# Optimization experiments

Measured on AMD Instinct MI355X. Metric: run time of the kernel, lower is better.

## Reference

```python
import jax, jax.numpy as jnp
import numpy as np


def _blur_kernel():
    # make_kernel([1,3,3,1]) -> outer product, normalized; * upsample_factor**2 (=4)
    k = np.array([1.0, 3.0, 3.0, 1.0], dtype=np.float32)
    k2 = np.outer(k, k)
    k2 /= k2.sum()
    k2 *= 4.0
    return jnp.asarray(k2)  # [4,4]


def setup_inputs() -> dict:
    key = jax.random.key(0)
    ks = jax.random.split(key, 6)
    B, Cin, Cout, H, W = 8, 128, 128, 128, 128
    style_dim, sd = 512, 32
    lin_out = Cin * (sd // 2) * (sd // 2)  # 128*16*16 = 32768
    return {
        "x": jax.random.normal(ks[0], (B, Cin, H, W), jnp.float32),
        "style": jax.random.normal(ks[1], (B, style_dim), jnp.float32),
        "weight": jax.random.normal(ks[2], (Cout, Cin, 3, 3), jnp.float32),
        "lin_w": jax.random.normal(ks[3], (lin_out, style_dim), jnp.float32),
        "lin_b": jnp.ones((lin_out,), jnp.float32),  # bias_init=1
        "convw_w": jax.random.normal(ks[4], (Cout, Cin, 3, 3), jnp.float32),
        "convw_b": jnp.zeros((Cout,), jnp.float32),
        "convb_w": jax.random.normal(ks[5], (Cout, Cin, 3, 3), jnp.float32),
        "convb_b": jnp.zeros((Cout,), jnp.float32),
    }


DN = ('NCHW', 'OIHW', 'NCHW')


def reference(x, style, weight, lin_w, lin_b, convw_w, convw_b, convb_w, convb_b):
    B, Cin, H, W = x.shape
    Cout, K = weight.shape[0], weight.shape[2]
    scale = 1.0 / np.sqrt(Cin * K * K)  # equalized-lr scale, fan_in = Cin*K*K
    w = scale * weight  # [Cout, Cin, K, K]; identical per-sample -> plain conv

    # F.conv_transpose2d(stride=2, padding=0) == dilated conv with flipped kernel
    out = jax.lax.conv_general_dilated(
        x, jnp.flip(w, (2, 3)), (1, 1), [(K - 1, K - 1)] * 2,
        lhs_dilation=(2, 2), dimension_numbers=DN)  # [B, Cout, 2H+1, 2W+1]

    # upfirdn2d blur with pad=(1,1): depthwise conv with flipped 4x4 kernel
    bk = _blur_kernel()
    bw = jnp.tile(jnp.flip(bk, (0, 1))[None, None], (Cout, 1, 1, 1))  # [Cout,1,4,4]
    out = jax.lax.conv_general_dilated(
        out, bw, (1, 1), [(1, 1), (1, 1)], feature_group_count=Cout,
        dimension_numbers=DN)  # [B, Cout, 2H, 2W]

    # InstanceNorm2d(affine=False), eps=1e-5, biased variance
    mu = out.mean((2, 3), keepdims=True)
    var = out.var((2, 3), keepdims=True)
    out = (out - mu) * jax.lax.rsqrt(var + 1e-5)
    Ho, Wo = out.shape[2], out.shape[3]

    # spatial_modulation_shared: EqualLinear (fused_lrelu) + View
    half = int(round(np.sqrt(lin_w.shape[0] // Cin)))  # spatial_dim // 2
    sd = 2 * half
    lscale = 1.0 / np.sqrt(style.shape[1])
    s = style @ (lin_w * lscale).T
    s = jax.nn.leaky_relu(s + lin_b, 0.2) * np.sqrt(2.0)  # fused_leaky_relu
    smap = s.reshape(B, Cin, half, half)
    # nn.Upsample(scale_factor=2, mode='nearest')
    smap = jnp.repeat(jnp.repeat(smap, 2, axis=2), 2, axis=3)  # [B,Cin,sd,sd]

    # two EqualConv2d(Cin, Cout, 3, padding=1)
    cscale = 1.0 / np.sqrt(Cin * 9)
    sw = jax.lax.conv_general_dilated(smap, convw_w * cscale, (1, 1),
                                      [(1, 1), (1, 1)], dimension_numbers=DN)
    sw = sw + convw_b[None, :, None, None]
    sb = jax.lax.conv_general_dilated(smap, convb_w * cscale, (1, 1),
                                      [(1, 1), (1, 1)], dimension_numbers=DN)
    sb = sb + convb_b[None, :, None, None]

    # F.interpolate(mode='nearest') to (Ho, Wo)
    hi = jnp.arange(Ho) * sd // Ho
    wi = jnp.arange(Wo) * sd // Wo
    sw = sw[:, :, hi][:, :, :, wi]
    sb = sb[:, :, hi][:, :, :, wi]

    return out * (1.0 + 0.3 * sw) + 0.3 * sb
```

## Files before the change

kernel.cpp:

```cpp
#include <hip/hip_runtime.h>
#include <cstdint>

#define SCALE_MAIN 0.029462782549439483f
#define LSCALE     0.044194173824159223f
#define CSCALE     0.029462782549439483f

typedef __attribute__((ext_vector_type(8))) short bf16x8;
typedef __attribute__((ext_vector_type(4))) float f32x4;
typedef __attribute__((ext_vector_type(2))) unsigned int u32x2;
typedef __attribute__((ext_vector_type(4))) unsigned int u32x4;

static __device__ __forceinline__ float lrelu_s2(float v) {
  return (v > 0.f ? v : 0.2f * v) * 1.4142135623730951f;
}
static __device__ __forceinline__ unsigned short f2bf(float f) {
  unsigned int u = __builtin_bit_cast(unsigned int, f);
  u += 0x7FFFu + ((u >> 16) & 1u);
  return (unsigned short)(u >> 16);
}
static __device__ __forceinline__ float s2f(unsigned short s) {
  return __builtin_bit_cast(float, (unsigned int)s << 16);
}
static __device__ __forceinline__ float lo16(unsigned int v) {
  return __builtin_bit_cast(float, v << 16);
}
static __device__ __forceinline__ float hi16(unsigned int v) {
  return __builtin_bit_cast(float, v & 0xFFFF0000u);
}

__global__ __launch_bounds__(256) void prep_all(
    const float* __restrict__ weight, const float* __restrict__ cw_w,
    const float* __restrict__ cb_w, const float* __restrict__ x,
    const float* __restrict__ style, const float* __restrict__ lin_w,
    const float* __restrict__ lin_b, short* __restrict__ kbu,
    short* __restrict__ kb2, unsigned short* __restrict__ xt,
    unsigned short* __restrict__ smap_bf) {
  int bid = blockIdx.x;
  int t = threadIdx.x;
  if (bid < 2048) {
    int idx = bid * 256 + t;
    int j   = idx & 7;
    int co  = (idx >> 3) & 255;
    int kc  = (idx >> 11) & 63;
    int par = idx >> 17;
    int k = kc * 8 + j;
    int t2 = k >> 7, ci = k & 127;
    int dy2 = t2 >> 1, dx2 = t2 & 1;
    int ph = par >> 1, pw = par & 1;
    const float* wsrc = (co < 128)
        ? cw_w + ((size_t)co * 128 + ci) * 9
        : cb_w + ((size_t)(co - 128) * 128 + ci) * 9;
    float acc = 0.f;
    #pragma unroll
    for (int kh = 0; kh < 3; ++kh) {
      bool okh = dy2 == 0 ? (ph == 0 ? kh == 0 : kh <= 1)
                          : (ph == 0 ? kh >= 1 : kh == 2);
      if (!okh) continue;
      #pragma unroll
      for (int kw = 0; kw < 3; ++kw) {
        bool okw = dx2 == 0 ? (pw == 0 ? kw == 0 : kw <= 1)
                            : (pw == 0 ? kw >= 1 : kw == 2);
        if (okw) acc += wsrc[kh * 3 + kw];
      }
    }
    kb2[idx] = (short)f2bf(acc * CSCALE);
  } else if (bid < 2624) {
    int idx2 = (bid - 2048) * 256 + t;
    int j    = idx2 & 7;
    int co   = (idx2 >> 3) & 127;
    int ksub = (idx2 >> 10) & 3;
    int s    = (idx2 >> 12) & 3;
    int tp   = idx2 >> 14;
    int ci = s * 32 + ksub * 8 + j;
    int wr = (tp == 0 || tp == 1 || tp == 4) ? 2
           : (tp >= 6) ? 1 : 0;
    int wc = (tp == 0 || tp == 2 || tp == 6) ? 2
           : (tp == 4 || tp == 5 || tp == 8) ? 1 : 0;
    float v = weight[((size_t)(co * 128 + ci)) * 9 + wr * 3 + wc] * SCALE_MAIN;
    kbu[idx2] = (short)f2bf(v);
  } else if (bid < 3648) {
    int q = bid - 2624;
    int y = q & 127, b = q >> 7;
    __shared__ unsigned short tl[128 * 134];
    #pragma unroll 4
    for (int i = 0; i < 16; ++i) {
      int c = t + i * 256;
      int ci = c >> 5, x4 = c & 31;
      f32x4 v = *(const f32x4*)(x + (size_t)(b * 128 + ci) * 16384 + y * 128 + x4 * 4);
      unsigned int* dst = (unsigned int*)(tl + ci * 134 + x4 * 4);
      dst[0] = (unsigned int)f2bf(v.x) | ((unsigned int)f2bf(v.y) << 16);
      dst[1] = (unsigned int)f2bf(v.z) | ((unsigned int)f2bf(v.w) << 16);
    }
    __syncthreads();
    #pragma unroll 2
    for (int i = 0; i < 8; ++i) {
      int c = t + i * 256;
      int xcol = c >> 4, sub = c & 15;
      unsigned short u[8];
      #pragma unroll
      for (int j = 0; j < 8; ++j) u[j] = tl[(sub * 8 + j) * 134 + xcol];
      u32x4 o;
      o.x = (unsigned int)u[0] | ((unsigned int)u[1] << 16);
      o.y = (unsigned int)u[2] | ((unsigned int)u[3] << 16);
      o.z = (unsigned int)u[4] | ((unsigned int)u[5] << 16);
      o.w = (unsigned int)u[6] | ((unsigned int)u[7] << 16);
      *(u32x4*)(xt + ((size_t)(b * 128 + y) * 128 + xcol) * 128 + sub * 8) = o;
    }
  } else {
    int wid = t >> 6, lane = t & 63;
    int gw = (bid - 3648) * 4 + wid;
    const float4* st4 = (const float4*)style;
    float s[8][8];
    #pragma unroll
    for (int b = 0; b < 8; ++b) {
      float4 a0 = st4[b * 128 + lane * 2];
      float4 a1 = st4[b * 128 + lane * 2 + 1];
      s[b][0] = a0.x; s[b][1] = a0.y; s[b][2] = a0.z; s[b][3] = a0.w;
      s[b][4] = a1.x; s[b][5] = a1.y; s[b][6] = a1.z; s[b][7] = a1.w;
    }
    for (int rr = 0; rr < 16; ++rr) {
      int j = gw * 16 + rr;
      const float4* wp = (const float4*)(lin_w + (size_t)j * 512);
      float4 w0 = wp[lane * 2], w1 = wp[lane * 2 + 1];
      float acc[8];
      #pragma unroll
      for (int b = 0; b < 8; ++b) {
        acc[b] = w0.x * s[b][0] + w0.y * s[b][1] + w0.z * s[b][2] + w0.w * s[b][3]
               + w1.x * s[b][4] + w1.y * s[b][5] + w1.z * s[b][6] + w1.w * s[b][7];
      }
      #pragma unroll
      for (int m = 32; m; m >>= 1) {
        #pragma unroll
        for (int b = 0; b < 8; ++b) acc[b] += __shfl_xor(acc[b], m, 64);
      }
      if (lane == 0) {
        float bias = lin_b[j];
        int ci = j >> 8, sp = j & 255;
        #pragma unroll
        for (int b = 0; b < 8; ++b)
          smap_bf[(size_t)(b * 256 + sp) * 128 + ci] =
              f2bf(lrelu_s2(acc[b] * LSCALE + bias));
      }
    }
  }
}

__global__ __launch_bounds__(512, 2) void modconv_kernel(
    const unsigned short* __restrict__ smap_bf, const short* __restrict__ kb2,
    const float* __restrict__ cw_b, const float* __restrict__ cb_b,
    float* __restrict__ swp) {
  extern __shared__ __align__(16) char dsm[];
  int par = blockIdx.x, b = blockIdx.y;
  int ph = par >> 1, pw = par & 1;
  int t = threadIdx.x, lane = t & 63, w = t >> 6;
  int q = w >> 1, ch = w & 1;
  int m15 = lane & 15, ksub = lane >> 4;

  for (int c = t; c < 4624; c += 512) {
    int s = c >> 4, cch = c & 15;
    int rr = s / 17, cc = s - rr * 17;
    int gr = rr - 1 + ph, gc = cc - 1 + pw;
    u32x4 v = {0u, 0u, 0u, 0u};
    if ((unsigned)gr < 16u && (unsigned)gc < 16u)
      v = *(const u32x4*)(smap_bf + ((size_t)(b * 256 + gr * 16 + gc) * 128 + cch * 8));
    int phys = (cch + s) & 15;
    *(u32x4*)(dsm + s * 256 + phys * 16) = v;
  }
  __syncthreads();

  const bf16x8* kbv = (const bf16x8*)kb2;
  f32x4 acc[4][8];
  #pragma unroll
  for (int i = 0; i < 4; ++i)
  #pragma unroll
  for (int j = 0; j < 8; ++j) acc[i][j] = (f32x4){0.f, 0.f, 0.f, 0.f};

  for (int s = 0; s < 16; ++s) {
    int t2 = s >> 2, dy2 = t2 >> 1, dx2 = t2 & 1;
    int cch = (s & 3) * 4 + ksub;
    bf16x8 av[4];
    #pragma unroll
    for (int mf = 0; mf < 4; ++mf) {
      int i = q * 4 + mf;
      int ssp = (i + dy2) * 17 + (m15 + dx2);
      int phys = (cch + ssp) & 15;
      av[mf] = *(const bf16x8*)(dsm + ssp * 256 + phys * 16);
    }
    #pragma unroll
    for (int nf = 0; nf < 8; ++nf) {
      bf16x8 bv = kbv[(size_t)((par * 64 + s * 4 + ksub) * 256 + ch * 128 + nf * 16 + m15)];
      #pragma unroll
      for (int mf = 0; mf < 4; ++mf)
        acc[mf][nf] = __builtin_amdgcn_mfma_f32_16x16x32_bf16(av[mf], bv, acc[mf][nf], 0, 0, 0);
    }
  }

  int jbase = ksub * 4;
  #pragma unroll
  for (int nf = 0; nf < 8; ++nf) {
    int co = ch * 128 + nf * 16 + m15;
    float bias = (co < 128) ? cw_b[co] : cb_b[co - 128];
    #pragma unroll
    for (int mf = 0; mf < 4; ++mf) {
      int i = q * 4 + mf;
      #pragma unroll
      for (int r = 0; r < 4; ++r) {
        int px = i * 16 + jbase + r;
        swp[((size_t)(b * 256 + co) * 4 + par) * 256 + px] = acc[mf][nf][r] + bias;
      }
    }
  }
}

__global__ __launch_bounds__(256, 2) void convt_kernel(
    const unsigned short* __restrict__ xt, const short* __restrict__ kbu,
    unsigned short* __restrict__ out1) {
  __shared__ __align__(16) char smem[26112];
  int cg = blockIdx.x, rp = blockIdx.y, b = blockIdx.z;
  int t = threadIdx.x, lane = t & 63, w = t >> 6;
  int m15 = lane & 15, ksub = lane >> 4;
  int pl = (w + cg + rp) & 3;
  int tstart = (pl == 0) ? 0 : 2 + 2 * pl;
  int nst = 16 >> ((pl + 1) >> 1);

  const char* xtc = (const char*)xt;
  for (int c = t; c < 1632; c += 256) {
    int spos = c >> 4, sub = c & 15;
    int lr = spos / 34, lc = spos - lr * 34;
    int y = 2 * rp - 1 + lr, xg = 32 * cg - 1 + lc;
    f32x4 v = {0.f, 0.f, 0.f, 0.f};
    if ((unsigned)y < 128u && (unsigned)xg < 128u)
      v = *(const f32x4*)(xtc + ((size_t)((b * 128 + y) * 128 + xg)) * 256 + sub * 16);
    int phys = (sub & 8) | ((sub ^ spos) & 7);
    *(f32x4*)(smem + spos * 256 + phys * 16) = v;
  }
  __syncthreads();

  const bf16x8* kbv = (const bf16x8*)kbu;
  f32x4 acc[4][8];
  #pragma unroll
  for (int i = 0; i < 4; ++i)
  #pragma unroll
  for (int j = 0; j < 8; ++j) acc[i][j] = (f32x4){0.f, 0.f, 0.f, 0.f};

  auto LD = [&](int s, bf16x8* av, bf16x8* bv) {
    int tap = tstart + (s >> 2);
    int du = -((0x13 >> tap) & 1);
    int dv = -((0x45 >> tap) & 1);
    int cc = s & 3;
    int c = cc * 4 + ksub;
    #pragma unroll
    for (int mf = 0; mf < 4; ++mf) {
      int spos = ((mf >> 1) + du + 1) * 34 + (mf & 1) * 16 + m15 + dv + 1;
      int phys = (c & 8) | ((c ^ spos) & 7);
      av[mf] = *(const bf16x8*)(smem + spos * 256 + phys * 16);
    }
    int bb = tap * 2048 + cc * 512 + ksub * 128 + m15;
    #pragma unroll
    for (int nf = 0; nf < 8; ++nf) bv[nf] = kbv[bb + nf * 16];
  };
  auto MM = [&](bf16x8* av, bf16x8* bv) {
    __builtin_amdgcn_s_setprio(1);
    #pragma unroll
    for (int nf = 0; nf < 8; ++nf)
    #pragma unroll
    for (int mf = 0; mf < 4; ++mf)
      acc[mf][nf] = __builtin_amdgcn_mfma_f32_16x16x32_bf16(av[mf], bv[nf], acc[mf][nf], 0, 0, 0);
    __builtin_amdgcn_s_setprio(0);
  };

  bf16x8 aA[4], bA[8], aB[4], bB[8];
  LD(0, aA, bA);
  for (int s = 0; s + 2 <= nst; s += 2) {
    LD(s + 1, aB, bB);
    MM(aA, bA);
    if (s + 2 < nst) LD(s + 2, aA, bA);
    MM(aB, bB);
  }

  __syncthreads();
  float* eps = (float*)smem;
  int t63 = t & 63, wpl = t >> 6;
  #pragma unroll
  for (int nf = 0; nf < 8; ++nf) {
    #pragma unroll
    for (int mf = 0; mf < 4; ++mf)
    #pragma unroll
    for (int r = 0; r < 4; ++r)
      eps[(pl * 64 + mf * 16 + ksub * 4 + r) * 17 + m15] = acc[mf][nf][r];
    __syncthreads();
    #pragma unroll
    for (int k = 0; k < 4; ++k) {
      int slot = k * 64 + t63;
      int co16 = slot >> 4, pr = (slot >> 3) & 1, ch = slot & 7;
      float v0 = eps[(wpl * 64 + pr * 32 + ch * 4 + 0) * 17 + co16];
      float v1 = eps[(wpl * 64 + pr * 32 + ch * 4 + 1) * 17 + co16];
      float v2 = eps[(wpl * 64 + pr * 32 + ch * 4 + 2) * 17 + co16];
      float v3 = eps[(wpl * 64 + pr * 32 + ch * 4 + 3) * 17 + co16];
      u32x2 o;
      o.x = (unsigned int)f2bf(v0) | ((unsigned int)f2bf(v1) << 16);
      o.y = (unsigned int)f2bf(v2) | ((unsigned int)f2bf(v3) << 16);
      int co = nf * 16 + co16;
      int r = 2 * rp + pr;
      size_t ob = (((size_t)(b * 4 + wpl) * 128 + co) * 130 + r) * 132
                + 32 * cg + ch * 4;
      if (cg < 4 || ch == 0) *(u32x2*)(out1 + ob) = o;
    }
    __syncthreads();
  }
}

template <int PASS>
__global__ __launch_bounds__(256) void blur_kernel(
    const unsigned short* __restrict__ out1, float* __restrict__ part,
    const float* __restrict__ swp, float* __restrict__ dout) {
  __shared__ unsigned short S[4][18][132];
  __shared__ float T[32][132];
  __shared__ float lsw[4][32], lsb[4][32];
  __shared__ float msh[2];
  __shared__ float rb2[8];
  int g = blockIdx.x, co = blockIdx.y, b = blockIdx.z;
  int t = threadIdx.x, lane = t & 63, wid = t >> 6;
  int bc = b * 128 + co;

  if (PASS == 1) {
    if (t == 0) {
      float a1 = 0.f, a2 = 0.f;
      #pragma unroll
      for (int i = 0; i < 8; ++i) {
        a1 += part[((size_t)bc * 8 + i) * 2];
        a2 += part[((size_t)bc * 8 + i) * 2 + 1];
      }
      float mean = a1 * (1.f / 65536.f);
      float var = a2 * (1.f / 65536.f) - mean * mean;
      msh[0] = mean; msh[1] = rsqrtf(var + 1e-5f);
    }
    {
      int which = t >> 7;
      int par = (t >> 5) & 3;
      int idx = t & 31;
      int hrow = idx >> 4, wcol = idx & 15;
      int px2 = (2 * g + hrow) * 16 + wcol;
      float v = swp[((size_t)(b * 256 + which * 128 + co) * 4 + par) * 256 + px2];
      if (which == 0) lsw[par][idx] = v; else lsb[par][idx] = v;
    }
  }

  int rbase = 16 * g - 1;
  for (int i = t; i < 2376; i += 256) {
    int pl = i / 594; int rem = i - pl * 594;
    int lr = rem / 33; int lc8 = rem - lr * 33;
    int r = rbase + lr;
    u32x2 v = {0u, 0u};
    if (r >= 0)
      v = *(const u32x2*)(out1 + ((size_t)((b * 4 + pl) * 128 + co) * 130 + r) * 132 + lc8 * 4);
    *(u32x2*)(&S[0][0][0] + (pl * 18 + lr) * 132 + lc8 * 4) = v;
  }
  if (t < 32) T[t][0] = 0.f;
  __syncthreads();

  float mean = 0.f, rstd = 0.f;
  if (PASS == 1) { mean = msh[0]; rstd = msh[1]; }
  float s1 = 0.f, s2 = 0.f;

  #pragma unroll
  for (int half = 0; half < 2; ++half) {
    if (half == 1) __syncthreads();
    if (t < 130) {
      int pw = (t >= 65) ? 1 : 0;
      int pc2 = t - 65 * pw;
      const unsigned int* E = (const unsigned int*)&S[pw][0][0] + pc2;
      const unsigned int* O = (const unsigned int*)&S[2 + pw][0][0] + pc2;
      float* Tr = &T[0][0] + pw * 132 + 2 * pc2 + 1;
      #pragma unroll
      for (int k = 0; k < 16; ++k) {
        int hl = half * 16 + k;
        int lrb = (hl + 1) >> 1;
        float v0, v1;
        if (hl & 1) {
          unsigned int e0 = E[lrb * 66],        o0 = O[lrb * 66];
          unsigned int e1 = E[(lrb + 1) * 66],  o1 = O[(lrb + 1) * 66];
          v0 = (lo16(e0) + lo16(o1)) + 3.f * (lo16(o0) + lo16(e1));
          v1 = (hi16(e0) + hi16(o1)) + 3.f * (hi16(o0) + hi16(e1));
        } else {
          unsigned int o0 = O[lrb * 66];
          unsigned int e1 = E[(lrb + 1) * 66],  o1 = O[(lrb + 1) * 66];
          unsigned int e2 = E[(lrb + 2) * 66];
          v0 = (lo16(o0) + lo16(e2)) + 3.f * (lo16(e1) + lo16(o1));
          v1 = (hi16(o0) + hi16(e2)) + 3.f * (hi16(e1) + hi16(o1));
        }
        Tr[k * 264] = v0;
        Tr[k * 264 + 1] = v1;
      }
    }
    __syncthreads();
    {
      int n = t & 127, hh = t >> 7;
      #pragma unroll
      for (int k = 0; k < 8; ++k) {
        int klocal = k * 2 + hh;
        const float* T0 = &T[klocal * 2][0];
        const float* T1 = &T[klocal * 2 + 1][0];
        float t0n = T0[n], t0n1 = T0[n + 1], t0n2 = T0[n + 2];
        float t1n = T1[n], t1n1 = T1[n + 1], t1n2 = T1[n + 2];
        float ve = ((t1n + t0n2) + 3.f * (t0n1 + t1n1)) * 0.0625f;
        float vo = ((t0n1 + t1n2) + 3.f * (t1n1 + t0n2)) * 0.0625f;
        if (PASS == 0) {
          s1 += ve + vo; s2 += ve * ve + vo * vo;
        } else {
          int hl = half * 16 + klocal;
          int h = 32 * g + hl;
          int par = ((klocal >> 3) & 1) * 2 + ((n >> 2) & 1);
          int lidx = half * 16 + (n >> 3);
          float msw = lsw[par][lidx], msb = lsb[par][lidx];
          float f1 = (1.f + 0.3f * msw) * rstd;
          float f0 = 0.3f * msb - mean * f1;
          float2 o = make_float2(ve * f1 + f0, vo * f1 + f0);
          *(float2*)(dout + ((size_t)bc * 256 + h) * 256 + 2 * n) = o;
        }
      }
    }
  }

  if (PASS == 0) {
    #pragma unroll
    for (int m = 32; m; m >>= 1) { s1 += __shfl_xor(s1, m, 64); s2 += __shfl_xor(s2, m, 64); }
    if (lane == 0) { rb2[wid * 2] = s1; rb2[wid * 2 + 1] = s2; }
    __syncthreads();
    if (t == 0) {
      part[((size_t)bc * 8 + g) * 2]     = rb2[0] + rb2[2] + rb2[4] + rb2[6];
      part[((size_t)bc * 8 + g) * 2 + 1] = rb2[1] + rb2[3] + rb2[5] + rb2[7];
    }
  }
}

extern "C" void kernel_launch(void* const* d_in, const int* in_sizes, int n_in,
                              void* d_out, int out_size, void* d_ws, size_t ws_size,
                              hipStream_t stream) {
  const float* x      = (const float*)d_in[0];
  const float* style  = (const float*)d_in[1];
  const float* weight = (const float*)d_in[2];
  const float* lin_w  = (const float*)d_in[3];
  const float* lin_b  = (const float*)d_in[4];
  const float* cw_w   = (const float*)d_in[5];
  const float* cw_b   = (const float*)d_in[6];
  const float* cb_w   = (const float*)d_in[7];
  const float* cb_b   = (const float*)d_in[8];
  float* out = (float*)d_out;
  char* ws = (char*)d_ws;

  short*          kbu     = (short*)(ws);
  short*          kb2     = (short*)(ws + 294912);
  unsigned short* xt      = (unsigned short*)(ws + 1343488);
  unsigned short* smap_bf = (unsigned short*)(ws + 34897920);
  float*          swp     = (float*)(ws + 35422208);
  float*          part    = (float*)(ws + 43810816);
  unsigned short* out1    = (unsigned short*)(ws + 43941888);

  prep_all<<<dim3(4160), dim3(256), 0, stream>>>(
      weight, cw_w, cb_w, x, style, lin_w, lin_b, kbu, kb2, xt, smap_bf);
  modconv_kernel<<<dim3(4, 8), dim3(512), 73984, stream>>>(smap_bf, kb2, cw_b, cb_b, swp);
  convt_kernel<<<dim3(5, 65, 8), dim3(256), 0, stream>>>(xt, kbu, out1);
  blur_kernel<0><<<dim3(8, 128, 8), dim3(256), 0, stream>>>(out1, part, swp, out);
  blur_kernel<1><<<dim3(8, 128, 8), dim3(256), 0, stream>>>(out1, part, swp, out);
}
```

Measured before the change: 372.2 us.

## Register-tile blur: each thread computes 4x8 outputs from registers without shared intermediate

Rewrites the separable blur stage so each thread loads a small window of the bf16 parity planes from shared memory into registers and computes both vertical and horizontal blur taps for a 4-row by 8-column output tile. This removes the float intermediate shared buffer, the extra barriers between passes, and the idle threads in the first pass. The shared layout becomes row-major with interleaved planes and padding, loads are widened, and outputs are written as 16-byte vectors. It raises register pressure and the window indexing is subtle.

```diff
diff --git a/kernel.cpp b/kernel.cpp
--- a/kernel.cpp
+++ b/kernel.cpp
@@ -18,15 +18,13 @@
   u += 0x7FFFu + ((u >> 16) & 1u);
   return (unsigned short)(u >> 16);
 }
-static __device__ __forceinline__ float s2f(unsigned short s) {
-  return __builtin_bit_cast(float, (unsigned int)s << 16);
-}
 static __device__ __forceinline__ float lo16(unsigned int v) {
   return __builtin_bit_cast(float, v << 16);
 }
 static __device__ __forceinline__ float hi16(unsigned int v) {
   return __builtin_bit_cast(float, v & 0xFFFF0000u);
 }
+#define EX(arr, rel) (((rel) & 1) ? lo16((arr)[((rel) + 1) >> 1]) : hi16((arr)[((rel) + 1) >> 1]))
 
 __global__ __launch_bounds__(256) void prep_all(
     const float* __restrict__ weight, const float* __restrict__ cw_w,
@@ -314,8 +312,7 @@
 __global__ __launch_bounds__(256) void blur_kernel(
     const unsigned short* __restrict__ out1, float* __restrict__ part,
     const float* __restrict__ swp, float* __restrict__ dout) {
-  __shared__ unsigned short S[4][18][132];
-  __shared__ float T[32][132];
+  __shared__ unsigned short S[18][4][144];
   __shared__ float lsw[4][32], lsb[4][32];
   __shared__ float msh[2];
   __shared__ float rb2[8];
@@ -347,78 +344,97 @@
   }
 
   int rbase = 16 * g - 1;
-  for (int i = t; i < 2376; i += 256) {
-    int pl = i / 594; int rem = i - pl * 594;
-    int lr = rem / 33; int lc8 = rem - lr * 33;
+  for (int i = t; i < 1152; i += 256) {
+    int rid = i >> 4, ch = i & 15;
+    int lr = rid >> 2, pl = rid & 3;
+    int r = rbase + lr;
+    u32x2 v0 = {0u, 0u}, v1 = {0u, 0u};
+    if (r >= 0) {
+      const unsigned short* src =
+          out1 + ((size_t)((b * 4 + pl) * 128 + co) * 130 + r) * 132 + ch * 8;
+      v0 = *(const u32x2*)(src);
+      v1 = *(const u32x2*)(src + 4);
+    }
+    *(u32x2*)(&S[lr][pl][8 + ch * 8]) = v0;
+    *(u32x2*)(&S[lr][pl][12 + ch * 8]) = v1;
+  }
+  if (t < 72) {
+    int lr = t >> 2, pl = t & 3;
     int r = rbase + lr;
     u32x2 v = {0u, 0u};
     if (r >= 0)
-      v = *(const u32x2*)(out1 + ((size_t)((b * 4 + pl) * 128 + co) * 130 + r) * 132 + lc8 * 4);
-    *(u32x2*)(&S[0][0][0] + (pl * 18 + lr) * 132 + lc8 * 4) = v;
-  }
-  if (t < 32) T[t][0] = 0.f;
+      v = *(const u32x2*)(out1 + ((size_t)((b * 4 + pl) * 128 + co) * 130 + r) * 132 + 128);
+    *(u32x2*)(&S[lr][pl][136]) = v;
+  }
+  if (t >= 128 && t < 200) {
+    int q = t - 128;
+    *(unsigned int*)(&S[q >> 2][q & 3][6]) = 0u;
+  }
   __syncthreads();
 
   float mean = 0.f, rstd = 0.f;
   if (PASS == 1) { mean = msh[0]; rstd = msh[1]; }
+
+  int rg = t >> 5, cg = t & 31;
+  int sr = 2 * rg;
+  unsigned int Eu[2][3][4], Ou[2][4][4];
+  #pragma unroll
+  for (int cp = 0; cp < 2; ++cp) {
+    #pragma unroll
+    for (int rr = 0; rr < 3; ++rr) {
+      const unsigned int* p = (const unsigned int*)&S[sr + 1 + rr][cp][0];
+      #pragma unroll
+      for (int j = 0; j < 4; ++j) Eu[cp][rr][j] = p[2 * cg + 3 + j];
+    }
+    #pragma unroll
+    for (int rr = 0; rr < 4; ++rr) {
+      const unsigned int* p = (const unsigned int*)&S[sr + rr][2 + cp][0];
+      #pragma unroll
+      for (int j = 0; j < 4; ++j) Ou[cp][rr][j] = p[2 * cg + 3 + j];
+    }
+  }
+
   float s1 = 0.f, s2 = 0.f;
-
-  #pragma unroll
-  for (int half = 0; half < 2; ++half) {
-    if (half == 1) __syncthreads();
-    if (t < 130) {
-      int pw = (t >= 65) ? 1 : 0;
-      int pc2 = t - 65 * pw;
-      const unsigned int* E = (const unsigned int*)&S[pw][0][0] + pc2;
-      const unsigned int* O = (const unsigned int*)&S[2 + pw][0][0] + pc2;
-      float* Tr = &T[0][0] + pw * 132 + 2 * pc2 + 1;
-      #pragma unroll
-      for (int k = 0; k < 16; ++k) {
-        int hl = half * 16 + k;
-        int lrb = (hl + 1) >> 1;
-        float v0, v1;
-        if (hl & 1) {
-          unsigned int e0 = E[lrb * 66],        o0 = O[lrb * 66];
-          unsigned int e1 = E[(lrb + 1) * 66],  o1 = O[(lrb + 1) * 66];
-          v0 = (lo16(e0) + lo16(o1)) + 3.f * (lo16(o0) + lo16(e1));
-          v1 = (hi16(e0) + hi16(o1)) + 3.f * (hi16(o0) + hi16(e1));
-        } else {
-          unsigned int o0 = O[lrb * 66];
-          unsigned int e1 = E[(lrb + 1) * 66],  o1 = O[(lrb + 1) * 66];
-          unsigned int e2 = E[(lrb + 2) * 66];
-          v0 = (lo16(o0) + lo16(e2)) + 3.f * (lo16(e1) + lo16(o1));
-          v1 = (hi16(o0) + hi16(e2)) + 3.f * (hi16(e1) + hi16(o1));
-        }
-        Tr[k * 264] = v0;
-        Tr[k * 264 + 1] = v1;
-      }
-    }
-    __syncthreads();
-    {
-      int n = t & 127, hh = t >> 7;
-      #pragma unroll
-      for (int k = 0; k < 8; ++k) {
-        int klocal = k * 2 + hh;
-        const float* T0 = &T[klocal * 2][0];
-        const float* T1 = &T[klocal * 2 + 1][0];
-        float t0n = T0[n], t0n1 = T0[n + 1], t0n2 = T0[n + 2];
-        float t1n = T1[n], t1n1 = T1[n + 1], t1n2 = T1[n + 2];
-        float ve = ((t1n + t0n2) + 3.f * (t0n1 + t1n1)) * 0.0625f;
-        float vo = ((t0n1 + t1n2) + 3.f * (t1n1 + t0n2)) * 0.0625f;
-        if (PASS == 0) {
-          s1 += ve + vo; s2 += ve * ve + vo * vo;
-        } else {
-          int hl = half * 16 + klocal;
-          int h = 32 * g + hl;
-          int par = ((klocal >> 3) & 1) * 2 + ((n >> 2) & 1);
-          int lidx = half * 16 + (n >> 3);
-          float msw = lsw[par][lidx], msb = lsb[par][lidx];
-          float f1 = (1.f + 0.3f * msw) * rstd;
-          float f0 = 0.3f * msb - mean * f1;
-          float2 o = make_float2(ve * f1 + f0, vo * f1 + f0);
-          *(float2*)(dout + ((size_t)bc * 256 + h) * 256 + 2 * n) = o;
-        }
-      }
+  #pragma unroll
+  for (int k = 0; k < 4; ++k) {
+    const int a = (k + 1) >> 1;
+    float Tc[2][6];
+    #pragma unroll
+    for (int cp = 0; cp < 2; ++cp)
+    #pragma unroll
+    for (int rel = 0; rel < 6; ++rel) {
+      float v;
+      if ((k & 1) == 0)
+        v = EX(Ou[cp][a], rel) + 3.f * EX(Eu[cp][a], rel)
+          + 3.f * EX(Ou[cp][a + 1], rel) + EX(Eu[cp][a + 1], rel);
+      else
+        v = EX(Eu[cp][a - 1], rel) + 3.f * EX(Ou[cp][a], rel)
+          + 3.f * EX(Eu[cp][a], rel) + EX(Ou[cp][a + 1], rel);
+      Tc[cp][rel] = v;
+    }
+    float o8[8];
+    #pragma unroll
+    for (int i = 0; i < 4; ++i) {
+      float ve = ((Tc[1][i] + Tc[0][i + 2]) + 3.f * (Tc[0][i + 1] + Tc[1][i + 1])) * 0.0625f;
+      float vo = ((Tc[0][i + 1] + Tc[1][i + 2]) + 3.f * (Tc[1][i + 1] + Tc[0][i + 2])) * 0.0625f;
+      if (PASS == 0) {
+        s1 += ve + vo; s2 += ve * ve + vo * vo;
+      } else {
+        o8[2 * i] = ve; o8[2 * i + 1] = vo;
+      }
+    }
+    if (PASS == 1) {
+      int hl = 4 * rg + k;
+      int h = 32 * g + hl;
+      int par = ((hl >> 3) & 1) * 2 + (cg & 1);
+      int lidx = ((hl >> 4) & 1) * 16 + (cg >> 1);
+      float f1 = (1.f + 0.3f * lsw[par][lidx]) * rstd;
+      float f0 = 0.3f * lsb[par][lidx] - mean * f1;
+      f32x4 oA = {o8[0] * f1 + f0, o8[1] * f1 + f0, o8[2] * f1 + f0, o8[3] * f1 + f0};
+      f32x4 oB = {o8[4] * f1 + f0, o8[5] * f1 + f0, o8[6] * f1 + f0, o8[7] * f1 + f0};
+      float* op = dout + ((size_t)bc * 256 + h) * 256 + 8 * cg;
+      *(f32x4*)(op) = oA;
+      *(f32x4*)(op + 4) = oB;
     }
   }
 
```

Result: faster. 343.8 us (-7.6%).
